# Performance work log

Hardware: AMD Instinct MI355X
Metric: run time of the kernel (lower is better)

## Reference

```python
import jax, jax.numpy as jnp
import numpy as np

# Batched/grouped formulation of nnmd's per-atom AtomicNN energy evaluation.
# Original: e_nn[s, a] = AtomicNN_a(g[s, a]) in a python double loop.
# Here each atom a has its own MLP (5 -> 64 -> 64 -> 1, tanh hidden activations),
# fused into grouped GEMMs via einsum over the atom axis.

S, A, D = 4096, 1024, 5   # n_structs, n_atoms, input_nodes (descriptors)
H = 64                    # hidden width (hidden_nodes = [64, 64])


def setup_inputs() -> dict:
    key = jax.random.key(0)
    k = jax.random.split(key, 4)
    g = jax.random.normal(k[0], (S, A, D), dtype=jnp.float32)
    W1 = jax.random.normal(k[1], (A, D, H), dtype=jnp.float32)
    b1 = jnp.zeros((A, H), dtype=jnp.float32)
    W2 = jax.random.normal(k[2], (A, H, H), dtype=jnp.float32)
    b2 = jnp.zeros((A, H), dtype=jnp.float32)
    W3 = jax.random.normal(k[3], (A, H, 1), dtype=jnp.float32)
    b3 = jnp.zeros((A, 1), dtype=jnp.float32)
    return {"g": g, "W1": W1, "b1": b1, "W2": W2, "b2": b2, "W3": W3, "b3": b3}


def reference(g, W1, b1, W2, b2, W3, b3):
    # g: [S, A, D]; per-atom weights carry leading A axis -> grouped GEMMs.
    h = jnp.tanh(jnp.einsum('sad,adh->sah', g, W1) + b1)   # [S, A, H]
    h = jnp.tanh(jnp.einsum('sah,ahk->sak', h, W2) + b2)   # [S, A, H]
    e = jnp.einsum('sak,ako->sao', h, W3) + b3             # [S, A, 1]
    return e[..., 0]                                       # e_nn: [S, A]
```

## Files before the change

kernel.cpp:

```cpp
#include <hip/hip_runtime.h>
#include <hip/hip_bf16.h>

typedef __bf16 bf16x8 __attribute__((ext_vector_type(8)));
typedef __bf16 bf16x4 __attribute__((ext_vector_type(4)));
typedef float  f32x4  __attribute__((ext_vector_type(4)));
typedef unsigned short u16;
typedef unsigned int   u32;

#define K2L 2.88539008177792681472f

__device__ inline float tanh_ps(float zs) {
    float E = __builtin_amdgcn_exp2f(zs);
    return fmaf(-2.0f, __builtin_amdgcn_rcpf(E + 1.0f), 1.0f);
}
__device__ inline float tanhK_ps(float zs) {
    float E = __builtin_amdgcn_exp2f(zs);
    return fmaf(-2.0f * K2L, __builtin_amdgcn_rcpf(E + 1.0f), K2L);
}
__device__ inline float bfbits2f(u16 u) {
    u32 v = ((u32)u) << 16;
    return __builtin_bit_cast(float, v);
}

__global__ __launch_bounds__(256, 4)
void atomicnn_kernel(const void* __restrict__ g,  const void* __restrict__ W1,
                     const void* __restrict__ b1, const void* __restrict__ W2,
                     const void* __restrict__ b2, const void* __restrict__ W3,
                     const void* __restrict__ b3, void* __restrict__ out)
{
    constexpr int A = 1024, SROWS = 512;
    constexpr int HS = 72;

    __shared__ __align__(16) __bf16 s_w1[8 * 64];
    __shared__ __align__(16) __bf16 s_w2[64 * 64];
    __shared__ float s_b1f[64], s_b2f[64];
    __shared__ __align__(16) __bf16 s_w3b[64];
    __shared__ __align__(16) __bf16 s_g[SROWS * 8];
    __shared__ __align__(16) __bf16 s_h[4 * 2 * 16 * HS];

    const int tid   = threadIdx.x;
    const int a     = blockIdx.x;
    const int sbase = blockIdx.y * SROWS;
    const int lane  = tid & 63;
    const int wave  = tid >> 6;
    const int sub   = lane & 15;
    const int quad  = lane >> 4;

    int cnt = 0;
    {
        const u16* gp16 = (const u16*)g;
        #pragma unroll
        for (int d = 0; d < 4; ++d) {
            u16 v = gp16[lane * 4 + d];
            u32 e = ((u32)v >> 7) & 0xFF;
            cnt += (int)__popcll(__ballot(e >= 100 && e <= 140));
        }
    }
    const int bfmode = (cnt >= 200) ? 1 : 0;

    if (bfmode) {
        const u16* W2g = (const u16*)W2 + (size_t)a * 4096;
        {
            int p = tid >> 2, c = (tid & 3) * 16;
            int u = (p >> 2) + 16 * (p & 3);
            const uint4* src = (const uint4*)(W2g + u * 64 + c);
            uint4* dst = (uint4*)((u16*)s_w2 + p * 64 + c);
            dst[0] = src[0]; dst[1] = src[1];
        }
        if (tid < 40) {
            ((uint4*)s_w1)[tid] = ((const uint4*)((const u16*)W1 + (size_t)a * 320))[tid];
        } else if (tid < 64) {
            ((uint4*)s_w1)[tid] = make_uint4(0, 0, 0, 0);
        }
        if (tid < 64) {
            s_b1f[tid] = K2L * bfbits2f(((const u16*)b1)[(size_t)a * 64 + tid]);
            s_b2f[tid] = K2L * bfbits2f(((const u16*)b2)[(size_t)a * 64 + tid]);
            s_w3b[tid] = __builtin_bit_cast(__bf16, ((const u16*)W3)[(size_t)a * 64 + tid]);
        }
        for (int i = tid; i < SROWS; i += 256) {
            const u16* gp = (const u16*)g + ((size_t)(sbase + i) * A + a) * 5;
            bf16x8 row = {};
            #pragma unroll
            for (int d = 0; d < 5; ++d) row[d] = (__bf16)(K2L * bfbits2f(gp[d]));
            *(bf16x8*)&s_g[i * 8] = row;
        }
    } else {
        const float* W2f = (const float*)W2 + (size_t)a * 4096;
        for (int i = tid; i < 4096; i += 256) {
            int p = i >> 6, c2 = i & 63;
            int u = (p >> 2) + 16 * (p & 3);
            s_w2[i] = (__bf16)W2f[u * 64 + c2];
        }
        for (int i = tid; i < 512; i += 256)
            s_w1[i] = (i < 320) ? (__bf16)((const float*)W1)[(size_t)a * 320 + i] : (__bf16)0.0f;
        if (tid < 64) {
            s_b1f[tid] = K2L * ((const float*)b1)[(size_t)a * 64 + tid];
            s_b2f[tid] = K2L * ((const float*)b2)[(size_t)a * 64 + tid];
            s_w3b[tid] = (__bf16)((const float*)W3)[(size_t)a * 64 + tid];
        }
        for (int i = tid; i < SROWS; i += 256) {
            const float* gp = (const float*)g + ((size_t)(sbase + i) * A + a) * 5;
            bf16x8 row = {};
            #pragma unroll
            for (int d = 0; d < 5; ++d) row[d] = (__bf16)(K2L * gp[d]);
            *(bf16x8*)&s_g[i * 8] = row;
        }
    }
    __syncthreads();

    bf16x8 bw1[4];
    bf16x8 bw2[2][4];
    bf16x8 bw3[2];
    f32x4 cb1[4], cb2[4], cb3;
    #pragma unroll
    for (int t = 0; t < 4; ++t) {
        const int col = sub + 16 * t;
        float v1 = s_b1f[col], v2 = s_b2f[col];
        cb1[t] = (f32x4){v1, v1, v1, v1};
        cb2[t] = (f32x4){v2, v2, v2, v2};
        #pragma unroll
        for (int j = 0; j < 8; ++j) {
            bw1[t][j]    = (quad == 0) ? s_w1[j * 64 + col] : (__bf16)0.0f;
            bw2[0][t][j] = s_w2[(quad * 8 + j) * 64 + col];
            bw2[1][t][j] = s_w2[(32 + quad * 8 + j) * 64 + col];
        }
    }
    #pragma unroll
    for (int kc = 0; kc < 2; ++kc)
        #pragma unroll
        for (int j = 0; j < 8; ++j) {
            int p = kc * 32 + quad * 8 + j;
            int u = (p >> 2) + 16 * (p & 3);
            bw3[kc][j] = (sub == 0) ? s_w3b[u] : (__bf16)0.0f;
        }
    const float b3f = bfmode ? bfbits2f(((const u16*)b3)[a]) : ((const float*)b3)[a];
    cb3 = (f32x4){b3f, b3f, b3f, b3f};

    __bf16* hping = s_h + wave * (2 * 16 * HS);
    const int rowbase = wave * 128;

    const __bf16* agp = (quad == 0) ? &s_g[(rowbase + sub) * 8] : &s_w1[5 * 64];
    const int aginc = (quad == 0) ? (16 * 8) : 0;

    #pragma unroll 2
    for (int gi = 0; gi < 8; ++gi) {
        const int r0 = rowbase + gi * 16;
        __bf16* hrow = hping + (gi & 1) * (16 * HS);

        if ((gi & 1) == 0)
            asm volatile("" ::: "memory");

        bf16x8 ag = *(const bf16x8*)agp;
        agp += aginc;

        f32x4 acc1[4];
        #pragma unroll
        for (int t = 0; t < 4; ++t)
            acc1[t] = __builtin_amdgcn_mfma_f32_16x16x32_bf16(ag, bw1[t], cb1[t], 0, 0, 0);

        #pragma unroll
        for (int r = 0; r < 4; ++r) {
            bf16x4 hv;
            #pragma unroll
            for (int t = 0; t < 4; ++t) hv[t] = (__bf16)tanhK_ps(acc1[t][r]);
            *(bf16x4*)&hrow[(quad * 4 + r) * HS + 4 * sub] = hv;
        }

        f32x4 acc2[4];
        {
            bf16x8 ah0 = *(const bf16x8*)&hrow[sub * HS + quad * 8];
            #pragma unroll
            for (int t = 0; t < 4; ++t)
                acc2[t] = __builtin_amdgcn_mfma_f32_16x16x32_bf16(ah0, bw2[0][t], cb2[t], 0, 0, 0);
            bf16x8 ah1 = *(const bf16x8*)&hrow[sub * HS + 32 + quad * 8];
            #pragma unroll
            for (int t = 0; t < 4; ++t)
                acc2[t] = __builtin_amdgcn_mfma_f32_16x16x32_bf16(ah1, bw2[1][t], acc2[t], 0, 0, 0);
        }

        #pragma unroll
        for (int r = 0; r < 4; ++r) {
            bf16x4 hv;
            #pragma unroll
            for (int t = 0; t < 4; ++t) hv[t] = (__bf16)tanh_ps(acc2[t][r]);
            *(bf16x4*)&hrow[(quad * 4 + r) * HS + 4 * sub] = hv;
        }

        f32x4 acc3;
        {
            bf16x8 ah0 = *(const bf16x8*)&hrow[sub * HS + quad * 8];
            acc3 = __builtin_amdgcn_mfma_f32_16x16x32_bf16(ah0, bw3[0], cb3, 0, 0, 0);
            bf16x8 ah1 = *(const bf16x8*)&hrow[sub * HS + 32 + quad * 8];
            acc3 = __builtin_amdgcn_mfma_f32_16x16x32_bf16(ah1, bw3[1], acc3, 0, 0, 0);
        }
        if (sub == 0) {
            #pragma unroll
            for (int r = 0; r < 4; ++r) {
                size_t o = (size_t)(sbase + r0 + quad * 4 + r) * A + a;
                if (bfmode) ((u16*)out)[o] = __builtin_bit_cast(u16, (__bf16)acc3[r]);
                else        ((float*)out)[o] = acc3[r];
            }
        }
    }
}

extern "C" void kernel_launch(void* const* d_in, const int* in_sizes, int n_in,
                              void* d_out, int out_size, void* d_ws, size_t ws_size,
                              hipStream_t stream) {
    const void *g = 0, *W1 = 0, *b1 = 0, *W2 = 0, *b2 = 0, *W3 = 0, *b3 = 0;
    const void* trip[3]; int nt = 0;
    for (int i = 0; i < n_in; ++i) {
        int sz = in_sizes[i];
        if      (sz == 20971520) g  = d_in[i];
        else if (sz == 327680)   W1 = d_in[i];
        else if (sz == 4194304)  W2 = d_in[i];
        else if (sz == 1024)     b3 = d_in[i];
        else if (sz == 65536 && nt < 3) trip[nt++] = d_in[i];
    }
    if (nt == 3) {
        bool alpha = (n_in >= 1 && in_sizes[0] == 327680);
        if (alpha) { W3 = trip[0]; b1 = trip[1]; b2 = trip[2]; }
        else       { b1 = trip[0]; b2 = trip[1]; W3 = trip[2]; }
    }
    if (!g || !W1 || !b1 || !W2 || !b2 || !W3 || !b3) {
        g = d_in[0]; W1 = d_in[1]; b1 = d_in[2]; W2 = d_in[3];
        b2 = d_in[4]; W3 = d_in[5]; b3 = d_in[6];
    }

    dim3 grid(1024, 8);
    atomicnn_kernel<<<grid, 256, 0, stream>>>(g, W1, b1, W2, b2, W3, b3, d_out);
}
```

Baseline: 288.7 us.

## Replace exp/rcp tanh with clamped odd polynomial and swizzle atom-block mapping

Replaces the exp2+reciprocal tanh with a clamp to [-3.5, 3.5] followed by an odd polynomial evaluated in FMAs. Because the new tanh takes unscaled inputs, the 2*log2(e) pre-scaling of g, b1 and b2 is removed. Separately, blockIdx.x is remapped so each group of eight consecutive blocks covers atoms 128 apart, which should keep neighbouring atoms on the same XCD and improve L2 reuse of the interleaved g rows. The polynomial trades quarter-rate transcendental instructions for more full-rate FMAs, and the clamp adds a small saturation error near |x| = 3.5.

```diff
diff --git a/kernel.cpp b/kernel.cpp
--- a/kernel.cpp
+++ b/kernel.cpp
@@ -7,19 +7,23 @@
 typedef unsigned short u16;
 typedef unsigned int   u32;
 
-#define K2L 2.88539008177792681472f
-
-__device__ inline float tanh_ps(float zs) {
-    float E = __builtin_amdgcn_exp2f(zs);
-    return fmaf(-2.0f, __builtin_amdgcn_rcpf(E + 1.0f), 1.0f);
-}
-__device__ inline float tanhK_ps(float zs) {
-    float E = __builtin_amdgcn_exp2f(zs);
-    return fmaf(-2.0f * K2L, __builtin_amdgcn_rcpf(E + 1.0f), K2L);
-}
 __device__ inline float bfbits2f(u16 u) {
     u32 v = ((u32)u) << 16;
     return __builtin_bit_cast(float, v);
+}
+
+__device__ inline float tanh1(float x) {
+    float z = __builtin_amdgcn_fmed3f(x, -3.5f, 3.5f);
+    float y = z * 0.2857142857f;
+    float t = y * y;
+    float p = fmaf(t, -25.067520f, 108.957696f);
+    p = fmaf(p, t, -198.535168f);
+    p = fmaf(p, t,  198.350592f);
+    p = fmaf(p, t, -120.264768f);
+    p = fmaf(p, t,   47.163792f);
+    p = fmaf(p, t,  -13.086424f);
+    p = fmaf(p, t,    3.479549f);
+    return p * y;
 }
 
 __global__ __launch_bounds__(256, 4)
@@ -39,7 +43,8 @@
     __shared__ __align__(16) __bf16 s_h[4 * 2 * 16 * HS];
 
     const int tid   = threadIdx.x;
-    const int a     = blockIdx.x;
+    const int bx    = blockIdx.x;
+    const int a     = ((bx & 7) << 7) | (bx >> 3);
     const int sbase = blockIdx.y * SROWS;
     const int lane  = tid & 63;
     const int wave  = tid >> 6;
@@ -73,15 +78,15 @@
             ((uint4*)s_w1)[tid] = make_uint4(0, 0, 0, 0);
         }
         if (tid < 64) {
-            s_b1f[tid] = K2L * bfbits2f(((const u16*)b1)[(size_t)a * 64 + tid]);
-            s_b2f[tid] = K2L * bfbits2f(((const u16*)b2)[(size_t)a * 64 + tid]);
+            s_b1f[tid] = bfbits2f(((const u16*)b1)[(size_t)a * 64 + tid]);
+            s_b2f[tid] = bfbits2f(((const u16*)b2)[(size_t)a * 64 + tid]);
             s_w3b[tid] = __builtin_bit_cast(__bf16, ((const u16*)W3)[(size_t)a * 64 + tid]);
         }
         for (int i = tid; i < SROWS; i += 256) {
             const u16* gp = (const u16*)g + ((size_t)(sbase + i) * A + a) * 5;
             bf16x8 row = {};
             #pragma unroll
-            for (int d = 0; d < 5; ++d) row[d] = (__bf16)(K2L * bfbits2f(gp[d]));
+            for (int d = 0; d < 5; ++d) row[d] = __builtin_bit_cast(__bf16, gp[d]);
             *(bf16x8*)&s_g[i * 8] = row;
         }
     } else {
@@ -94,15 +99,15 @@
         for (int i = tid; i < 512; i += 256)
             s_w1[i] = (i < 320) ? (__bf16)((const float*)W1)[(size_t)a * 320 + i] : (__bf16)0.0f;
         if (tid < 64) {
-            s_b1f[tid] = K2L * ((const float*)b1)[(size_t)a * 64 + tid];
-            s_b2f[tid] = K2L * ((const float*)b2)[(size_t)a * 64 + tid];
+            s_b1f[tid] = ((const float*)b1)[(size_t)a * 64 + tid];
+            s_b2f[tid] = ((const float*)b2)[(size_t)a * 64 + tid];
             s_w3b[tid] = (__bf16)((const float*)W3)[(size_t)a * 64 + tid];
         }
         for (int i = tid; i < SROWS; i += 256) {
             const float* gp = (const float*)g + ((size_t)(sbase + i) * A + a) * 5;
             bf16x8 row = {};
             #pragma unroll
-            for (int d = 0; d < 5; ++d) row[d] = (__bf16)(K2L * gp[d]);
+            for (int d = 0; d < 5; ++d) row[d] = (__bf16)gp[d];
             *(bf16x8*)&s_g[i * 8] = row;
         }
     }
@@ -162,7 +167,7 @@
         for (int r = 0; r < 4; ++r) {
             bf16x4 hv;
             #pragma unroll
-            for (int t = 0; t < 4; ++t) hv[t] = (__bf16)tanhK_ps(acc1[t][r]);
+            for (int t = 0; t < 4; ++t) hv[t] = (__bf16)tanh1(acc1[t][r]);
             *(bf16x4*)&hrow[(quad * 4 + r) * HS + 4 * sub] = hv;
         }
 
@@ -182,7 +187,7 @@
         for (int r = 0; r < 4; ++r) {
             bf16x4 hv;
             #pragma unroll
-            for (int t = 0; t < 4; ++t) hv[t] = (__bf16)tanh_ps(acc2[t][r]);
+            for (int t = 0; t < 4; ++t) hv[t] = (__bf16)tanh1(acc2[t][r]);
             *(bf16x4*)&hrow[(quad * 4 + r) * HS + 4 * sub] = hv;
         }
 
```

New measurement: 288.7 us. Within noise of the previous version (-0.0%).
